# Kernel optimization log

Hardware: AMD Instinct MI355X
Metric: run time of the kernel (lower is better)

The kernel has to match this reference:

```python
import jax, jax.numpy as jnp
import numpy as np

N_NODES = 50000
N_EDGES = 600000
D = 128
H_MLP = 256
N_LABELS = 10
EPS = 0.0  # tf_geometric GIN default eps


def _gin_layer(x, src, dst, W, b):
    # gather neighbor (source) features and sum-aggregate into destinations
    msg = x[src]                                   # [E, D] irregular gather
    agg = jax.ops.segment_sum(msg, dst, num_segments=N_NODES)  # [N, D]
    h = (1.0 + EPS) * x + agg                      # GIN sum update
    return jax.nn.relu(h @ W + b)                  # dense transform + relu


def setup_inputs() -> dict:
    key = jax.random.key(0)
    ks = jax.random.split(key, 8)
    x = jax.random.normal(ks[0], (N_NODES, D), dtype=jnp.float32)
    edge_index = jax.random.randint(ks[1], (2, N_EDGES), 0, N_NODES, dtype=jnp.int32)
    s = 1.0 / np.sqrt(D)
    W0 = jax.random.normal(ks[2], (D, D), dtype=jnp.float32) * s
    W1 = jax.random.normal(ks[3], (D, D), dtype=jnp.float32) * s
    W2 = jax.random.normal(ks[4], (D, D), dtype=jnp.float32) * s
    Wm1 = jax.random.normal(ks[5], (D, H_MLP), dtype=jnp.float32) * s
    Wm2 = jax.random.normal(ks[6], (H_MLP, N_LABELS), dtype=jnp.float32) * (1.0 / np.sqrt(H_MLP))
    return {
        'x': x, 'edge_index': edge_index,
        'W0': W0, 'b0': jnp.zeros((D,), jnp.float32),
        'W1': W1, 'b1': jnp.zeros((D,), jnp.float32),
        'W2': W2, 'b2': jnp.zeros((D,), jnp.float32),
        'Wm1': Wm1, 'bm1': jnp.zeros((H_MLP,), jnp.float32),
        'Wm2': Wm2, 'bm2': jnp.zeros((N_LABELS,), jnp.float32),
    }


def reference(x, edge_index, W0, b0, W1, b1, W2, b2, Wm1, bm1, Wm2, bm2):
    src, dst = edge_index[0], edge_index[1]
    h = _gin_layer(x, src, dst, W0, b0)
    h = _gin_layer(h, src, dst, W1, b1)
    h = _gin_layer(h, src, dst, W2, b2)
    # head: Flatten is identity on [N, D]; Dense(256, relu) -> Dense(num_labels)
    h = jax.nn.relu(h @ Wm1 + bm1)
    return h @ Wm2 + bm2  # [N, num_labels] logits
```

## Files before the change

kernel.cpp:

```cpp
#include <hip/hip_runtime.h>


typedef short short8 __attribute__((ext_vector_type(8)));
typedef float v4f __attribute__((ext_vector_type(4)));
typedef float v2f __attribute__((ext_vector_type(2)));

#define BCAP 1024
#define MAXB 1024

__device__ inline unsigned short f2bf(float f) {
  union { float f; unsigned int u; } c; c.f = f;
  unsigned int u = c.u;
  return (unsigned short)((u + 0x7fffu + ((u >> 16) & 1u)) >> 16);
}
__device__ inline float bfbits2f(unsigned int hi) {
  union { unsigned int u; float f; } c; c.u = hi; return c.f;
}
__device__ inline unsigned int pack2(float a, float b) {
  return (unsigned int)f2bf(a) | ((unsigned int)f2bf(b) << 16);
}
__device__ inline void add8(float* s, uint4 v) {
  s[0] += bfbits2f(v.x << 16); s[1] += bfbits2f(v.x & 0xffff0000u);
  s[2] += bfbits2f(v.y << 16); s[3] += bfbits2f(v.y & 0xffff0000u);
  s[4] += bfbits2f(v.z << 16); s[5] += bfbits2f(v.z & 0xffff0000u);
  s[6] += bfbits2f(v.w << 16); s[7] += bfbits2f(v.w & 0xffff0000u);
}
__device__ inline void addf8q(float* s, uint4 v) {
  v2f p;
  p = __builtin_amdgcn_cvt_pk_f32_fp8(v.x, false); s[0]  += p.x; s[1]  += p.y;
  p = __builtin_amdgcn_cvt_pk_f32_fp8(v.x, true);  s[2]  += p.x; s[3]  += p.y;
  p = __builtin_amdgcn_cvt_pk_f32_fp8(v.y, false); s[4]  += p.x; s[5]  += p.y;
  p = __builtin_amdgcn_cvt_pk_f32_fp8(v.y, true);  s[6]  += p.x; s[7]  += p.y;
  p = __builtin_amdgcn_cvt_pk_f32_fp8(v.z, false); s[8]  += p.x; s[9]  += p.y;
  p = __builtin_amdgcn_cvt_pk_f32_fp8(v.z, true);  s[10] += p.x; s[11] += p.y;
  p = __builtin_amdgcn_cvt_pk_f32_fp8(v.w, false); s[12] += p.x; s[13] += p.y;
  p = __builtin_amdgcn_cvt_pk_f32_fp8(v.w, true);  s[14] += p.x; s[15] += p.y;
}
__device__ inline unsigned char f2fp8(float v) {
  return (unsigned char)(__builtin_amdgcn_cvt_pk_fp8_f32(v, v, 0, false) & 0xff);
}
__device__ inline int wave_incl_scan_int(int v, int lane) {
#pragma unroll
  for (int off = 1; off < 64; off <<= 1) {
    int t = __shfl_up(v, off, 64);
    if (lane >= off) v += t;
  }
  return v;
}

__global__ __launch_bounds__(256) void prep_all(
    const float* __restrict__ W0, const float* __restrict__ W1, const float* __restrict__ W2,
    const float* __restrict__ Wm1, const float* __restrict__ Wm2,
    unsigned short* __restrict__ W0T, unsigned short* __restrict__ W1T,
    unsigned short* __restrict__ W2T, unsigned short* __restrict__ Wm1T,
    unsigned short* __restrict__ Wm2T,
    const float* __restrict__ x, unsigned short* __restrict__ xb,
    unsigned char* __restrict__ xq, int n8,
    int* __restrict__ bcnt) {
  int i = blockIdx.x * 256 + threadIdx.x;
  if (i < MAXB) bcnt[i] = 0;
  if (i < n8) {
    const float4* p = (const float4*)x;
    float4 a = p[2 * (size_t)i], b = p[2 * (size_t)i + 1];
    uint4 o;
    o.x = pack2(a.x, a.y); o.y = pack2(a.z, a.w);
    o.z = pack2(b.x, b.y); o.w = pack2(b.z, b.w);
    ((uint4*)xb)[i] = o;
    unsigned int lo = 0, hi = 0;
    lo = __builtin_amdgcn_cvt_pk_fp8_f32(a.x, a.y, lo, false);
    lo = __builtin_amdgcn_cvt_pk_fp8_f32(a.z, a.w, lo, true);
    hi = __builtin_amdgcn_cvt_pk_fp8_f32(b.x, b.y, hi, false);
    hi = __builtin_amdgcn_cvt_pk_fp8_f32(b.z, b.w, hi, true);
    uint2 q; q.x = lo; q.y = hi;
    ((uint2*)xq)[i] = q;
  }
  if (i < 49152) {
    int w = i / 16384, r = i % 16384;
    int frag = r >> 9, l = (r >> 3) & 63, j = r & 7;
    int kq = frag >> 3, nfr = frag & 7;
    int nn = nfr * 16 + (l & 15);
    int k  = kq * 32 + (l >> 4) * 8 + j;
    const float* W = (w == 0) ? W0 : (w == 1) ? W1 : W2;
    unsigned short* O = (w == 0) ? W0T : (w == 1) ? W1T : W2T;
    O[r] = f2bf(W[k * 128 + nn]);
  } else if (i < 49152 + 32768) {
    int r = i - 49152;
    int frag = r >> 9, l = (r >> 3) & 63, j = r & 7;
    int kq = frag >> 4, nfr = frag & 15;
    int nn = nfr * 16 + (l & 15);
    int k  = kq * 32 + (l >> 4) * 8 + j;
    Wm1T[r] = f2bf(Wm1[k * 256 + nn]);
  } else if (i < 49152 + 32768 + 4096) {
    int r = i - 49152 - 32768;
    int kq = r >> 9, l = (r >> 3) & 63, j = r & 7;
    int nn = l & 15;
    int k  = kq * 32 + (l >> 4) * 8 + j;
    Wm2T[r] = (nn < 10) ? f2bf(Wm2[k * 10 + nn]) : (unsigned short)0;
  }
}

__global__ __launch_bounds__(256) void bin_edges(
    const int* __restrict__ src, const int* __restrict__ dst, int E, int per,
    int* __restrict__ bcnt, int* __restrict__ bucketA, int nbuckets) {
  __shared__ int hist[MAXB];
  __shared__ int base[MAXB];
  const int tid = threadIdx.x;
  const int e0 = blockIdx.x * per;
  const int e1 = (e0 + per < E) ? e0 + per : E;
  for (int j = tid; j < nbuckets; j += 256) hist[j] = 0;
  __syncthreads();
  for (int i = e0 + tid; i < e1; i += 256) atomicAdd(&hist[dst[i] >> 6], 1);
  __syncthreads();
  for (int j = tid; j < nbuckets; j += 256) {
    int h = hist[j];
    base[j] = h ? atomicAdd(&bcnt[j], h) : 0;
  }
  __syncthreads();
  for (int i = e0 + tid; i < e1; i += 256) {
    int d = dst[i], s = src[i];
    int b = d >> 6;
    int r = atomicAdd(&base[b], 1);
    bucketA[(size_t)b * BCAP + r] = (s << 6) | (d & 63);
  }
}

__global__ __launch_bounds__(256) void sort_buckets(
    const int* __restrict__ bcnt, const int* __restrict__ bucketA,
    int* __restrict__ srcsS, int* __restrict__ boffs) {
  __shared__ int rawE[BCAP];
  __shared__ int hist[64], cur[64], offs[65];
  const int tid = threadIdx.x;
  const int b = blockIdx.x;
  const int cnt = bcnt[b];
  for (int i = tid; i < cnt; i += 256) rawE[i] = bucketA[(size_t)b * BCAP + i];
  if (tid < 64) hist[tid] = 0;
  __syncthreads();
  for (int i = tid; i < cnt; i += 256) atomicAdd(&hist[rawE[i] & 63], 1);
  __syncthreads();
  if (tid < 64) {
    int v = hist[tid];
    int incl = wave_incl_scan_int(v, tid);
    offs[tid] = incl - v;
    cur[tid] = incl - v;
    if (tid == 63) offs[64] = incl;
  }
  __syncthreads();
  for (int i = tid; i < cnt; i += 256) {
    int e = rawE[i];
    int p = atomicAdd(&cur[e & 63], 1);
    srcsS[(size_t)b * BCAP + p] = e >> 6;
  }
  if (tid < 65) boffs[b * 65 + tid] = offs[tid];
}

__global__ __launch_bounds__(256) void fused_layer(
    const unsigned short* __restrict__ Xb, const unsigned char* __restrict__ Xq,
    const int* __restrict__ bcnt,
    const int* __restrict__ srcsS, const int* __restrict__ boffs,
    const unsigned short* __restrict__ BT, const float* __restrict__ bias,
    unsigned char* __restrict__ Cq, int M) {
  __shared__ __align__(16) unsigned short As[64 * 136];
  __shared__ int srcS[BCAP];
  __shared__ int offs[65];
  const int tid = threadIdx.x;
  const int lane = tid & 63;
  const int b = blockIdx.x;
  const int blk = b * 64;
  const int cnt = bcnt[b];

  if (tid < 65) offs[tid] = boffs[b * 65 + tid];
  for (int i = tid; i < cnt; i += 256) srcS[i] = srcsS[(size_t)b * BCAP + i];
  __syncthreads();

  const int l = tid & 7, g = tid >> 3;
  const uint4* baseb = (const uint4*)Xb;
  const uint4* baseq = (const uint4*)Xq;
#pragma unroll
  for (int s2 = 0; s2 < 2; ++s2) {
    int nl = s2 * 32 + g;
    int node = blk + nl;
    float s[16] = {0, 0, 0, 0, 0, 0, 0, 0, 0, 0, 0, 0, 0, 0, 0, 0};
    if (node < M) {
      if (Xb) {
        add8(s, baseb[(size_t)node * 16 + l * 2]);
        add8(s + 8, baseb[(size_t)node * 16 + l * 2 + 1]);
      } else {
        addf8q(s, baseq[(size_t)node * 8 + l]);
      }
      int beg = offs[nl], c = offs[nl + 1] - beg;
      int j = 0;
      for (; j + 8 <= c; j += 8) {
        int i0 = srcS[beg + j + 0], i1 = srcS[beg + j + 1];
        int i2 = srcS[beg + j + 2], i3 = srcS[beg + j + 3];
        int i4 = srcS[beg + j + 4], i5 = srcS[beg + j + 5];
        int i6 = srcS[beg + j + 6], i7 = srcS[beg + j + 7];
        uint4 v0 = baseq[(size_t)i0 * 8 + l];
        uint4 v1 = baseq[(size_t)i1 * 8 + l];
        uint4 v2 = baseq[(size_t)i2 * 8 + l];
        uint4 v3 = baseq[(size_t)i3 * 8 + l];
        uint4 v4 = baseq[(size_t)i4 * 8 + l];
        uint4 v5 = baseq[(size_t)i5 * 8 + l];
        uint4 v6 = baseq[(size_t)i6 * 8 + l];
        uint4 v7 = baseq[(size_t)i7 * 8 + l];
        addf8q(s, v0); addf8q(s, v1); addf8q(s, v2); addf8q(s, v3);
        addf8q(s, v4); addf8q(s, v5); addf8q(s, v6); addf8q(s, v7);
      }
      if (j + 4 <= c) {
        int i0 = srcS[beg + j + 0], i1 = srcS[beg + j + 1];
        int i2 = srcS[beg + j + 2], i3 = srcS[beg + j + 3];
        uint4 v0 = baseq[(size_t)i0 * 8 + l];
        uint4 v1 = baseq[(size_t)i1 * 8 + l];
        uint4 v2 = baseq[(size_t)i2 * 8 + l];
        uint4 v3 = baseq[(size_t)i3 * 8 + l];
        addf8q(s, v0); addf8q(s, v1); addf8q(s, v2); addf8q(s, v3);
        j += 4;
      }
      if (j + 2 <= c) {
        int i0 = srcS[beg + j + 0], i1 = srcS[beg + j + 1];
        uint4 v0 = baseq[(size_t)i0 * 8 + l];
        uint4 v1 = baseq[(size_t)i1 * 8 + l];
        addf8q(s, v0); addf8q(s, v1);
        j += 2;
      }
      if (j < c) addf8q(s, baseq[(size_t)srcS[beg + j] * 8 + l]);
    }
    uint4 o0, o1;
    o0.x = pack2(s[0], s[1]);   o0.y = pack2(s[2], s[3]);
    o0.z = pack2(s[4], s[5]);   o0.w = pack2(s[6], s[7]);
    o1.x = pack2(s[8], s[9]);   o1.y = pack2(s[10], s[11]);
    o1.z = pack2(s[12], s[13]); o1.w = pack2(s[14], s[15]);
    *(uint4*)&As[nl * 136 + l * 16] = o0;
    *(uint4*)&As[nl * 136 + l * 16 + 8] = o1;
  }
  __syncthreads();

  const int w = tid >> 6;
  const int wm = w & 1, wn = w >> 1;
  const int l15 = lane & 15, quad = lane >> 4;
  const int mb = wm * 32, nb2 = wn * 64;

  v4f acc[2][4];
#pragma unroll
  for (int mf = 0; mf < 2; ++mf)
#pragma unroll
    for (int nf = 0; nf < 4; ++nf) acc[mf][nf] = (v4f)0.f;

#pragma unroll
  for (int k0 = 0; k0 < 128; k0 += 32) {
    const int kq = k0 >> 5;
    short8 a[2], bv[4];
#pragma unroll
    for (int mf = 0; mf < 2; ++mf)
      a[mf] = *(const short8*)&As[(mb + mf * 16 + l15) * 136 + k0 + quad * 8];
#pragma unroll
    for (int nf = 0; nf < 4; ++nf)
      bv[nf] = *(const short8*)(BT + (size_t)(kq * 8 + wn * 4 + nf) * 512 + lane * 8);
#pragma unroll
    for (int mf = 0; mf < 2; ++mf)
#pragma unroll
      for (int nf = 0; nf < 4; ++nf)
        acc[mf][nf] = __builtin_amdgcn_mfma_f32_16x16x32_bf16(a[mf], bv[nf], acc[mf][nf], 0, 0, 0);
  }

#pragma unroll
  for (int mf = 0; mf < 2; ++mf) {
#pragma unroll
    for (int r = 0; r < 4; ++r) {
      int grow = blk + mb + mf * 16 + quad * 4 + r;
      if (grow >= M) continue;
#pragma unroll
      for (int nf = 0; nf < 4; ++nf) {
        int gcol = nb2 + nf * 16 + l15;
        float v = fmaxf(acc[mf][nf][r] + bias[gcol], 0.f);
        Cq[(size_t)grow * 128 + gcol] = f2fp8(v);
      }
    }
  }
}

__global__ __launch_bounds__(256) void fused_l3_head(
    const unsigned char* __restrict__ Xq,
    const int* __restrict__ bcnt,
    const int* __restrict__ srcsS, const int* __restrict__ boffs,
    const unsigned short* __restrict__ W2T, const float* __restrict__ b2,
    const unsigned short* __restrict__ Wm1T, const float* __restrict__ bm1,
    const unsigned short* __restrict__ Wm2T, const float* __restrict__ bm2,
    float* __restrict__ out, int M, int NOUT) {
  __shared__ __align__(16) unsigned char lds[64 * 264 * 2];
  unsigned short* As = (unsigned short*)lds;
  int* srcS = (int*)(lds + 64 * 136 * 2);
  unsigned short* Hs = (unsigned short*)lds;
  __shared__ int offs[65];
  const int tid = threadIdx.x;
  const int lane = tid & 63;
  const int b = blockIdx.x;
  const int blk = b * 64;
  const int cnt = bcnt[b];

  if (tid < 65) offs[tid] = boffs[b * 65 + tid];
  for (int i = tid; i < cnt; i += 256) srcS[i] = srcsS[(size_t)b * BCAP + i];
  __syncthreads();

  const int l = tid & 7, g = tid >> 3;
  const uint4* baseq = (const uint4*)Xq;
#pragma unroll
  for (int s2 = 0; s2 < 2; ++s2) {
    int nl = s2 * 32 + g;
    int node = blk + nl;
    float s[16] = {0, 0, 0, 0, 0, 0, 0, 0, 0, 0, 0, 0, 0, 0, 0, 0};
    if (node < M) {
      addf8q(s, baseq[(size_t)node * 8 + l]);
      int beg = offs[nl], c = offs[nl + 1] - beg;
      int j = 0;
      for (; j + 8 <= c; j += 8) {
        int i0 = srcS[beg + j + 0], i1 = srcS[beg + j + 1];
        int i2 = srcS[beg + j + 2], i3 = srcS[beg + j + 3];
        int i4 = srcS[beg + j + 4], i5 = srcS[beg + j + 5];
        int i6 = srcS[beg + j + 6], i7 = srcS[beg + j + 7];
        uint4 v0 = baseq[(size_t)i0 * 8 + l];
        uint4 v1 = baseq[(size_t)i1 * 8 + l];
        uint4 v2 = baseq[(size_t)i2 * 8 + l];
        uint4 v3 = baseq[(size_t)i3 * 8 + l];
        uint4 v4 = baseq[(size_t)i4 * 8 + l];
        uint4 v5 = baseq[(size_t)i5 * 8 + l];
        uint4 v6 = baseq[(size_t)i6 * 8 + l];
        uint4 v7 = baseq[(size_t)i7 * 8 + l];
        addf8q(s, v0); addf8q(s, v1); addf8q(s, v2); addf8q(s, v3);
        addf8q(s, v4); addf8q(s, v5); addf8q(s, v6); addf8q(s, v7);
      }
      if (j + 4 <= c) {
        int i0 = srcS[beg + j + 0], i1 = srcS[beg + j + 1];
        int i2 = srcS[beg + j + 2], i3 = srcS[beg + j + 3];
        uint4 v0 = baseq[(size_t)i0 * 8 + l];
        uint4 v1 = baseq[(size_t)i1 * 8 + l];
        uint4 v2 = baseq[(size_t)i2 * 8 + l];
        uint4 v3 = baseq[(size_t)i3 * 8 + l];
        addf8q(s, v0); addf8q(s, v1); addf8q(s, v2); addf8q(s, v3);
        j += 4;
      }
      if (j + 2 <= c) {
        int i0 = srcS[beg + j + 0], i1 = srcS[beg + j + 1];
        uint4 v0 = baseq[(size_t)i0 * 8 + l];
        uint4 v1 = baseq[(size_t)i1 * 8 + l];
        addf8q(s, v0); addf8q(s, v1);
        j += 2;
      }
      if (j < c) addf8q(s, baseq[(size_t)srcS[beg + j] * 8 + l]);
    }
    uint4 o0, o1;
    o0.x = pack2(s[0], s[1]);   o0.y = pack2(s[2], s[3]);
    o0.z = pack2(s[4], s[5]);   o0.w = pack2(s[6], s[7]);
    o1.x = pack2(s[8], s[9]);   o1.y = pack2(s[10], s[11]);
    o1.z = pack2(s[12], s[13]); o1.w = pack2(s[14], s[15]);
    *(uint4*)&As[nl * 136 + l * 16] = o0;
    *(uint4*)&As[nl * 136 + l * 16 + 8] = o1;
  }
  __syncthreads();

  const int w = tid >> 6;
  const int wm = w & 1, wn = w >> 1;
  const int l15 = lane & 15, quad = lane >> 4;
  const int mb = wm * 32, nb2 = wn * 64;

  v4f acc[2][4];
#pragma unroll
  for (int mf = 0; mf < 2; ++mf)
#pragma unroll
    for (int nf = 0; nf < 4; ++nf) acc[mf][nf] = (v4f)0.f;

#pragma unroll
  for (int k0 = 0; k0 < 128; k0 += 32) {
    const int kq = k0 >> 5;
    short8 a[2], bv[4];
#pragma unroll
    for (int mf = 0; mf < 2; ++mf)
      a[mf] = *(const short8*)&As[(mb + mf * 16 + l15) * 136 + k0 + quad * 8];
#pragma unroll
    for (int nf = 0; nf < 4; ++nf)
      bv[nf] = *(const short8*)(W2T + (size_t)(kq * 8 + wn * 4 + nf) * 512 + lane * 8);
#pragma unroll
    for (int mf = 0; mf < 2; ++mf)
#pragma unroll
      for (int nf = 0; nf < 4; ++nf)
        acc[mf][nf] = __builtin_amdgcn_mfma_f32_16x16x32_bf16(a[mf], bv[nf], acc[mf][nf], 0, 0, 0);
  }
  __syncthreads();

#pragma unroll
  for (int mf = 0; mf < 2; ++mf)
#pragma unroll
    for (int r = 0; r < 4; ++r) {
      int row = mb + mf * 16 + quad * 4 + r;
#pragma unroll
      for (int nf = 0; nf < 4; ++nf) {
        int col = nb2 + nf * 16 + l15;
        As[row * 136 + col] = f2bf(fmaxf(acc[mf][nf][r] + b2[col], 0.f));
      }
    }
  __syncthreads();

  const int nbH = wn * 128;
  v4f acc2[2][8];
#pragma unroll
  for (int mf = 0; mf < 2; ++mf)
#pragma unroll
    for (int nf = 0; nf < 8; ++nf) acc2[mf][nf] = (v4f)0.f;

#pragma unroll
  for (int k0 = 0; k0 < 128; k0 += 32) {
    const int kq = k0 >> 5;
    short8 a[2];
#pragma unroll
    for (int mf = 0; mf < 2; ++mf)
      a[mf] = *(const short8*)&As[(mb + mf * 16 + l15) * 136 + k0 + quad * 8];
#pragma unroll
    for (int nf = 0; nf < 8; ++nf) {
      short8 bb = *(const short8*)(Wm1T + (size_t)(kq * 16 + wn * 8 + nf) * 512 + lane * 8);
#pragma unroll
      for (int mf = 0; mf < 2; ++mf)
        acc2[mf][nf] = __builtin_amdgcn_mfma_f32_16x16x32_bf16(a[mf], bb, acc2[mf][nf], 0, 0, 0);
    }
  }
  __syncthreads();

#pragma unroll
  for (int mf = 0; mf < 2; ++mf)
#pragma unroll
    for (int r = 0; r < 4; ++r) {
      int row = mb + mf * 16 + quad * 4 + r;
#pragma unroll
      for (int nf = 0; nf < 8; ++nf) {
        int col = nbH + nf * 16 + l15;
        Hs[row * 264 + col] = f2bf(fmaxf(acc2[mf][nf][r] + bm1[col], 0.f));
      }
    }
  __syncthreads();

  const int rowl = w * 16 + l15;
  v4f acc3 = (v4f)0.f;
#pragma unroll
  for (int k0 = 0; k0 < 256; k0 += 32)
    acc3 = __builtin_amdgcn_mfma_f32_16x16x32_bf16(
        *(const short8*)&Hs[rowl * 264 + k0 + quad * 8],
        *(const short8*)(Wm2T + (size_t)(k0 >> 5) * 512 + lane * 8), acc3, 0, 0, 0);
  float bb = (l15 < NOUT) ? bm2[l15] : 0.f;
#pragma unroll
  for (int r = 0; r < 4; ++r) {
    int grow = blk + w * 16 + quad * 4 + r;
    if (grow < M && l15 < NOUT) out[(size_t)grow * NOUT + l15] = acc3[r] + bb;
  }
}


extern "C" void kernel_launch(void* const* d_in, const int* in_sizes, int n_in,
                              void* d_out, int out_size, void* d_ws, size_t ws_size,
                              hipStream_t stream) {
  const float* x   = (const float*)d_in[0];
  const int*   ei  = (const int*)d_in[1];
  const float* W0  = (const float*)d_in[2];
  const float* b0  = (const float*)d_in[3];
  const float* W1  = (const float*)d_in[4];
  const float* b1  = (const float*)d_in[5];
  const float* W2  = (const float*)d_in[6];
  const float* b2  = (const float*)d_in[7];
  const float* Wm1 = (const float*)d_in[8];
  const float* bm1 = (const float*)d_in[9];
  const float* Wm2 = (const float*)d_in[10];
  const float* bm2 = (const float*)d_in[11];
  float* out = (float*)d_out;

  const int D = 128;
  const int N = in_sizes[0] / D;
  const int E = in_sizes[1] / 2;
  const int L = in_sizes[11];
  const int nb = (N + 63) / 64;

  const int* srcv = ei;
  const int* dstv = ei + E;

  char* ws = (char*)d_ws;
  size_t off = 0;
  auto alloc = [&](size_t bytes) -> void* {
    void* p = ws + off;
    off = (off + bytes + 255) & ~(size_t)255;
    return p;
  };
  int* bcnt    = (int*)alloc((size_t)MAXB * 4);
  int* bucketA = (int*)alloc((size_t)nb * BCAP * 4);
  int* srcsS   = (int*)alloc((size_t)nb * BCAP * 4);
  int* boffs   = (int*)alloc((size_t)nb * 65 * 4);
  unsigned short* xb   = (unsigned short*)alloc((size_t)N * 128 * 2);
  unsigned char*  xq   = (unsigned char*)alloc((size_t)N * 128);
  unsigned char*  h1q  = (unsigned char*)alloc((size_t)N * 128);
  unsigned char*  h2q  = (unsigned char*)alloc((size_t)N * 128);
  unsigned short* W0T  = (unsigned short*)alloc(128 * 128 * 2);
  unsigned short* W1T  = (unsigned short*)alloc(128 * 128 * 2);
  unsigned short* W2T  = (unsigned short*)alloc(128 * 128 * 2);
  unsigned short* Wm1T = (unsigned short*)alloc(256 * 128 * 2);
  unsigned short* Wm2T = (unsigned short*)alloc(16 * 256 * 2);
  (void)ws_size; (void)n_in; (void)out_size;

  const int tpb = 256;
  int n8 = N * 16;
  prep_all<<<dim3((n8 + tpb - 1) / tpb), dim3(tpb), 0, stream>>>(
      W0, W1, W2, Wm1, Wm2, W0T, W1T, W2T, Wm1T, Wm2T, x, xb, xq, n8, bcnt);

  const int nbin = 256;
  int per = (E + nbin - 1) / nbin;
  bin_edges<<<dim3(nbin), dim3(tpb), 0, stream>>>(srcv, dstv, E, per, bcnt, bucketA, nb);
  sort_buckets<<<dim3(nb), dim3(tpb), 0, stream>>>(bcnt, bucketA, srcsS, boffs);

  dim3 lgrid(nb);
  fused_layer<<<lgrid, dim3(tpb), 0, stream>>>(
      xb, xq, bcnt, srcsS, boffs, W0T, b0, h1q, N);
  fused_layer<<<lgrid, dim3(tpb), 0, stream>>>(
      nullptr, h1q, bcnt, srcsS, boffs, W1T, b1, h2q, N);
  fused_l3_head<<<lgrid, dim3(tpb), 0, stream>>>(
      h2q, bcnt, srcsS, boffs, W2T, b2, Wm1T, bm1, Wm2T, bm2, out, N, L);
}
```

Before: 202.6 us.

## Merge prep and edge binning into one launch, stage layer output through LDS

The weight/feature conversion kernel and the edge-binning kernel are combined into a single launch whose blocks branch on their index. Binning now uses more blocks (512 instead of 256), and the bucket counter is zeroed with a memset before the launch. Separately, fused_layer writes its fp8 outputs into shared memory first and then copies the tile to global memory as coalesced 16-byte stores instead of scattered byte stores. This saves a launch and improves write coalescing, at the cost of an extra memset call and two barriers.

```diff
diff --git a/kernel.cpp b/kernel.cpp
--- a/kernel.cpp
+++ b/kernel.cpp
@@ -7,6 +7,7 @@
 
 #define BCAP 1024
 #define MAXB 1024
+#define NBIN 512
 
 __device__ inline unsigned short f2bf(float f) {
   union { float f; unsigned int u; } c; c.f = f;
@@ -48,79 +49,78 @@
   return v;
 }
 
-__global__ __launch_bounds__(256) void prep_all(
+__global__ __launch_bounds__(256) void prep_bin(
     const float* __restrict__ W0, const float* __restrict__ W1, const float* __restrict__ W2,
     const float* __restrict__ Wm1, const float* __restrict__ Wm2,
     unsigned short* __restrict__ W0T, unsigned short* __restrict__ W1T,
     unsigned short* __restrict__ W2T, unsigned short* __restrict__ Wm1T,
     unsigned short* __restrict__ Wm2T,
     const float* __restrict__ x, unsigned short* __restrict__ xb,
-    unsigned char* __restrict__ xq, int n8,
-    int* __restrict__ bcnt) {
-  int i = blockIdx.x * 256 + threadIdx.x;
-  if (i < MAXB) bcnt[i] = 0;
-  if (i < n8) {
-    const float4* p = (const float4*)x;
-    float4 a = p[2 * (size_t)i], b = p[2 * (size_t)i + 1];
-    uint4 o;
-    o.x = pack2(a.x, a.y); o.y = pack2(a.z, a.w);
-    o.z = pack2(b.x, b.y); o.w = pack2(b.z, b.w);
-    ((uint4*)xb)[i] = o;
-    unsigned int lo = 0, hi = 0;
-    lo = __builtin_amdgcn_cvt_pk_fp8_f32(a.x, a.y, lo, false);
-    lo = __builtin_amdgcn_cvt_pk_fp8_f32(a.z, a.w, lo, true);
-    hi = __builtin_amdgcn_cvt_pk_fp8_f32(b.x, b.y, hi, false);
-    hi = __builtin_amdgcn_cvt_pk_fp8_f32(b.z, b.w, hi, true);
-    uint2 q; q.x = lo; q.y = hi;
-    ((uint2*)xq)[i] = q;
-  }
-  if (i < 49152) {
-    int w = i / 16384, r = i % 16384;
-    int frag = r >> 9, l = (r >> 3) & 63, j = r & 7;
-    int kq = frag >> 3, nfr = frag & 7;
-    int nn = nfr * 16 + (l & 15);
-    int k  = kq * 32 + (l >> 4) * 8 + j;
-    const float* W = (w == 0) ? W0 : (w == 1) ? W1 : W2;
-    unsigned short* O = (w == 0) ? W0T : (w == 1) ? W1T : W2T;
-    O[r] = f2bf(W[k * 128 + nn]);
-  } else if (i < 49152 + 32768) {
-    int r = i - 49152;
-    int frag = r >> 9, l = (r >> 3) & 63, j = r & 7;
-    int kq = frag >> 4, nfr = frag & 15;
-    int nn = nfr * 16 + (l & 15);
-    int k  = kq * 32 + (l >> 4) * 8 + j;
-    Wm1T[r] = f2bf(Wm1[k * 256 + nn]);
-  } else if (i < 49152 + 32768 + 4096) {
-    int r = i - 49152 - 32768;
-    int kq = r >> 9, l = (r >> 3) & 63, j = r & 7;
-    int nn = l & 15;
-    int k  = kq * 32 + (l >> 4) * 8 + j;
-    Wm2T[r] = (nn < 10) ? f2bf(Wm2[k * 10 + nn]) : (unsigned short)0;
-  }
-}
-
-__global__ __launch_bounds__(256) void bin_edges(
+    unsigned char* __restrict__ xq, int n8, int PB,
     const int* __restrict__ src, const int* __restrict__ dst, int E, int per,
     int* __restrict__ bcnt, int* __restrict__ bucketA, int nbuckets) {
   __shared__ int hist[MAXB];
   __shared__ int base[MAXB];
   const int tid = threadIdx.x;
-  const int e0 = blockIdx.x * per;
-  const int e1 = (e0 + per < E) ? e0 + per : E;
-  for (int j = tid; j < nbuckets; j += 256) hist[j] = 0;
-  __syncthreads();
-  for (int i = e0 + tid; i < e1; i += 256) atomicAdd(&hist[dst[i] >> 6], 1);
-  __syncthreads();
-  for (int j = tid; j < nbuckets; j += 256) {
-    int h = hist[j];
-    base[j] = h ? atomicAdd(&bcnt[j], h) : 0;
-  }
-  __syncthreads();
-  for (int i = e0 + tid; i < e1; i += 256) {
-    int d = dst[i], s = src[i];
-    int b = d >> 6;
-    int r = atomicAdd(&base[b], 1);
-    bucketA[(size_t)b * BCAP + r] = (s << 6) | (d & 63);
+  if (blockIdx.x < PB) {
+    int i = blockIdx.x * 256 + tid;
+    if (i < n8) {
+      const float4* p = (const float4*)x;
+      float4 a = p[2 * (size_t)i], b = p[2 * (size_t)i + 1];
+      uint4 o;
+      o.x = pack2(a.x, a.y); o.y = pack2(a.z, a.w);
+      o.z = pack2(b.x, b.y); o.w = pack2(b.z, b.w);
+      ((uint4*)xb)[i] = o;
+      unsigned int lo = 0, hi = 0;
+      lo = __builtin_amdgcn_cvt_pk_fp8_f32(a.x, a.y, lo, false);
+      lo = __builtin_amdgcn_cvt_pk_fp8_f32(a.z, a.w, lo, true);
+      hi = __builtin_amdgcn_cvt_pk_fp8_f32(b.x, b.y, hi, false);
+      hi = __builtin_amdgcn_cvt_pk_fp8_f32(b.z, b.w, hi, true);
+      uint2 q; q.x = lo; q.y = hi;
+      ((uint2*)xq)[i] = q;
+    }
+    if (i < 49152) {
+      int w = i / 16384, r = i % 16384;
+      int frag = r >> 9, l = (r >> 3) & 63, j = r & 7;
+      int kq = frag >> 3, nfr = frag & 7;
+      int nn = nfr * 16 + (l & 15);
+      int k  = kq * 32 + (l >> 4) * 8 + j;
+      const float* W = (w == 0) ? W0 : (w == 1) ? W1 : W2;
+      unsigned short* O = (w == 0) ? W0T : (w == 1) ? W1T : W2T;
+      O[r] = f2bf(W[k * 128 + nn]);
+    } else if (i < 49152 + 32768) {
+      int r = i - 49152;
+      int frag = r >> 9, l = (r >> 3) & 63, j = r & 7;
+      int kq = frag >> 4, nfr = frag & 15;
+      int nn = nfr * 16 + (l & 15);
+      int k  = kq * 32 + (l >> 4) * 8 + j;
+      Wm1T[r] = f2bf(Wm1[k * 256 + nn]);
+    } else if (i < 49152 + 32768 + 4096) {
+      int r = i - 49152 - 32768;
+      int kq = r >> 9, l = (r >> 3) & 63, j = r & 7;
+      int nn = l & 15;
+      int k  = kq * 32 + (l >> 4) * 8 + j;
+      Wm2T[r] = (nn < 10) ? f2bf(Wm2[k * 10 + nn]) : (unsigned short)0;
+    }
+  } else {
+    const int bb = blockIdx.x - PB;
+    const int e0 = bb * per;
+    const int e1 = (e0 + per < E) ? e0 + per : E;
+    for (int j = tid; j < nbuckets; j += 256) hist[j] = 0;
+    __syncthreads();
+    for (int i = e0 + tid; i < e1; i += 256) atomicAdd(&hist[dst[i] >> 6], 1);
+    __syncthreads();
+    for (int j = tid; j < nbuckets; j += 256) {
+      int h = hist[j];
+      base[j] = h ? atomicAdd(&bcnt[j], h) : 0;
+    }
+    __syncthreads();
+    for (int i = e0 + tid; i < e1; i += 256) {
+      int d = dst[i], s = src[i];
+      int b = d >> 6;
+      int r = atomicAdd(&base[b], 1);
+      bucketA[(size_t)b * BCAP + r] = (s << 6) | (d & 63);
+    }
   }
 }
 
@@ -261,20 +261,29 @@
       for (int nf = 0; nf < 4; ++nf)
         acc[mf][nf] = __builtin_amdgcn_mfma_f32_16x16x32_bf16(a[mf], bv[nf], acc[mf][nf], 0, 0, 0);
   }
-
-#pragma unroll
-  for (int mf = 0; mf < 2; ++mf) {
+  __syncthreads();
+
+  unsigned char* Cs = (unsigned char*)As;
+#pragma unroll
+  for (int mf = 0; mf < 2; ++mf)
 #pragma unroll
     for (int r = 0; r < 4; ++r) {
-      int grow = blk + mb + mf * 16 + quad * 4 + r;
-      if (grow >= M) continue;
+      int row = mb + mf * 16 + quad * 4 + r;
 #pragma unroll
       for (int nf = 0; nf < 4; ++nf) {
-        int gcol = nb2 + nf * 16 + l15;
-        float v = fmaxf(acc[mf][nf][r] + bias[gcol], 0.f);
-        Cq[(size_t)grow * 128 + gcol] = f2fp8(v);
-      }
-    }
+        int col = nb2 + nf * 16 + l15;
+        Cs[row * 128 + col] = f2fp8(fmaxf(acc[mf][nf][r] + bias[col], 0.f));
+      }
+    }
+  __syncthreads();
+  uint4* dst4 = (uint4*)(Cq + (size_t)blk * 128);
+  const uint4* s4 = (const uint4*)Cs;
+  if (blk + 64 <= M) {
+    dst4[tid] = s4[tid];
+    dst4[tid + 256] = s4[tid + 256];
+  } else {
+    for (int c2 = tid; c2 < 512; c2 += 256)
+      if (blk + (c2 >> 3) < M) dst4[c2] = s4[c2];
   }
 }
 
@@ -502,12 +511,13 @@
 
   const int tpb = 256;
   int n8 = N * 16;
-  prep_all<<<dim3((n8 + tpb - 1) / tpb), dim3(tpb), 0, stream>>>(
-      W0, W1, W2, Wm1, Wm2, W0T, W1T, W2T, Wm1T, Wm2T, x, xb, xq, n8, bcnt);
-
-  const int nbin = 256;
-  int per = (E + nbin - 1) / nbin;
-  bin_edges<<<dim3(nbin), dim3(tpb), 0, stream>>>(srcv, dstv, E, per, bcnt, bucketA, nb);
+  const int PB = (n8 + tpb - 1) / tpb;
+  int per = (E + NBIN - 1) / NBIN;
+
+  hipMemsetAsync(bcnt, 0, (size_t)MAXB * 4, stream);
+  prep_bin<<<dim3(PB + NBIN), dim3(tpb), 0, stream>>>(
+      W0, W1, W2, Wm1, Wm2, W0T, W1T, W2T, Wm1T, Wm2T,
+      x, xb, xq, n8, PB, srcv, dstv, E, per, bcnt, bucketA, nb);
   sort_buckets<<<dim3(nb), dim3(tpb), 0, stream>>>(bcnt, bucketA, srcsS, boffs);
 
   dim3 lgrid(nb);
```

Result: no change. 201.1 us (-0.8%).
